# Performance work log

Measured on AMD Instinct MI355X. Metric: run time of the kernel, lower is better.

Reference implementation:

```python
import jax, jax.numpy as jnp
import numpy as np

DY, DO, DI = 16, 256, 256
BS = 4096
EPS = 1e-6


def setup_inputs() -> dict:
    key = jax.random.key(0)
    k1, k2, k3, k4, k5 = jax.random.split(key, 5)
    k = 1.0 / float(np.sqrt(DY * DI))
    return {
        "x": jax.random.normal(k1, (DY * DI, BS), dtype=jnp.float32),
        "rms_params": jnp.ones((DY * DI,), dtype=jnp.float32)
        + 0.01 * jax.random.normal(k2, (DY * DI,), dtype=jnp.float32),
        "w_upper": jax.random.uniform(k3, (DY, DO, DI), minval=-k, maxval=k, dtype=jnp.float32),
        "w_lower": jax.random.uniform(k4, (DY, DO, DI), minval=-k, maxval=k, dtype=jnp.float32),
        "bias": jax.random.uniform(k5, (DY * DO,), minval=-k, maxval=k, dtype=jnp.float32),
    }


def reference(x, rms_params, w_upper, w_lower, bias):
    # x: (dy*di, bs) features-first layout, matching the torch op.
    dy, do, di = w_upper.shape
    bs = x.shape[1]
    # Per-column RMS factor (fc in the original op is shape (bs,)).
    fc = jax.lax.rsqrt(jnp.mean(x * x, axis=0) + EPS)  # (bs,)
    xn = x * rms_params[:, None] * fc[None, :]          # fused norm+scale
    xb = xn.reshape(dy, di, bs)
    # Dyadic structured matmul: upper acts on block d, lower on its paired
    # (reversed) block dy-1-d.
    up = jnp.einsum("doi,dib->dob", w_upper, xb)
    lo = jnp.einsum("doi,dib->dob", w_lower, xb[::-1])
    y = jax.nn.relu(up + lo + bias.reshape(dy, do, 1))
    return y.reshape(dy * do, bs)
```

## Files before the change

kernel.cpp:

```cpp
#include <hip/hip_runtime.h>

#define DYN 16
#define DON 256
#define DIN 256
#define BSN 4096
#define NF 4096
#define KTOT 512

typedef unsigned short u16;
typedef __attribute__((ext_vector_type(8))) short bf16x8;
typedef __attribute__((ext_vector_type(4))) float f32x4;
typedef __attribute__((ext_vector_type(4))) unsigned short u16x4;

static __device__ __forceinline__ u16 f2bf(float f) {
  unsigned u = __builtin_bit_cast(unsigned, f);
  u += 0x7fffu + ((u >> 16) & 1u);
  return (u16)(u >> 16);
}
static __device__ __forceinline__ float bf2f(u16 h) {
  unsigned u = ((unsigned)h) << 16;
  return __builtin_bit_cast(float, u);
}

__global__ __launch_bounds__(256) void k_pre(
    const float* __restrict__ x, const float* __restrict__ wu,
    const float* __restrict__ wl, const float* __restrict__ rms,
    u16* __restrict__ aprep, u16* __restrict__ xbf,
    float* __restrict__ partial) {
  __shared__ u16 tile[128 * 132];
  const int t = threadIdx.x;
  if (blockIdx.x < 1024) {
    int e = blockIdx.x * 256 + t;
    int row = e >> 6;
    int k0 = (e & 63) << 3;
    int d = row >> 8;
    const float* src;
    const float* rp;
    if (k0 < 256) {
      src = wu + (size_t)row * 256 + k0;
      rp  = rms + d * 256 + k0;
    } else {
      src = wl + (size_t)row * 256 + (k0 - 256);
      rp  = rms + (DYN - 1 - d) * 256 + (k0 - 256);
    }
    float4 s0 = *reinterpret_cast<const float4*>(src);
    float4 s1 = *reinterpret_cast<const float4*>(src + 4);
    float4 r0 = *reinterpret_cast<const float4*>(rp);
    float4 r1 = *reinterpret_cast<const float4*>(rp + 4);
    bf16x8 o;
    o[0] = (short)f2bf(s0.x * r0.x); o[1] = (short)f2bf(s0.y * r0.y);
    o[2] = (short)f2bf(s0.z * r0.z); o[3] = (short)f2bf(s0.w * r0.w);
    o[4] = (short)f2bf(s1.x * r1.x); o[5] = (short)f2bf(s1.y * r1.y);
    o[6] = (short)f2bf(s1.z * r1.z); o[7] = (short)f2bf(s1.w * r1.w);
    *reinterpret_cast<bf16x8*>(aprep + (size_t)row * KTOT + k0) = o;
    return;
  }
  const int bid = blockIdx.x - 1024;
  const int bt = bid & 31, ft = bid >> 5;
  const float* xb = x + (size_t)ft * 128 * BSN + bt * 128;
  const int frow = t >> 5, b4 = (t & 31) * 4;
  #pragma unroll
  for (int p = 0; p < 16; ++p) {
    int f = p * 8 + frow;
    float4 v = *reinterpret_cast<const float4*>(xb + (size_t)f * BSN + b4);
    u16x4 h;
    h[0] = f2bf(v.x); h[1] = f2bf(v.y); h[2] = f2bf(v.z); h[3] = f2bf(v.w);
    *reinterpret_cast<u16x4*>(&tile[f * 132 + b4]) = h;
  }
  __syncthreads();
  const int chunk = t & 15;
  const int bg = t >> 4;
  #pragma unroll
  for (int p = 0; p < 8; ++p) {
    int b = bg + p * 16;
    float s = 0.f;
    bf16x8 w;
    #pragma unroll
    for (int jj = 0; jj < 8; ++jj) {
      int j = (jj + chunk) & 7;
      u16 v = tile[(chunk * 8 + j) * 132 + b];
      float xv = bf2f(v);
      s += xv * xv;
      w[j] = (short)v;
    }
    *reinterpret_cast<bf16x8*>(
        xbf + (size_t)(bt * 128 + b) * NF + ft * 128 + chunk * 8) = w;
    #pragma unroll
    for (int m = 1; m < 16; m <<= 1) s += __shfl_xor(s, m, 64);
    if (chunk == 0) partial[ft * BSN + bt * 128 + b] = s;
  }
}

__global__ __launch_bounds__(512, 2) void k_gemm(
    const u16* __restrict__ aprep, const u16* __restrict__ xbf,
    const float* __restrict__ partial, const float* __restrict__ bias,
    float* __restrict__ out) {
  extern __shared__ char smem[];
  float* fcl = (float*)(smem + 98304);
  const int bid = blockIdx.x;
  const int dp = bid & 7;
  const int d = ((bid >> 3) & 1) ? (15 - dp) : dp;
  const int bt = bid >> 4;
  const int b0 = bt * 256;
  const int fr0 = d * 256;
  const int t = threadIdx.x;
  const int wave = t >> 6, lane = t & 63;
  const int lhi = lane >> 4, llo = lane & 15;
  const int wm = wave >> 2, wn = wave & 3;
  const int kmask = ((llo >> 1) & 7) << 4;

  f32x4 acc[8][4] = {};

  auto stage1 = [&](int slot, int kt, int op) {
    int j = op & 1;
    int c = j * 512 + t;
    int cl = c ^ ((c >> 3) & 7);
    int r = cl >> 2, kc = cl & 3;
    unsigned lbase = (unsigned)(slot * 32768 + (op >= 2 ? 16384 : 0) +
                                (j * 512 + wave * 64) * 16);
    const u16* g;
    if (op < 2) {
      int fbase = (kt < 8) ? (d * 256 + kt * 32)
                           : ((15 - d) * 256 + (kt - 8) * 32);
      g = xbf + (size_t)(b0 + r) * NF + fbase + kc * 8;
    } else {
      g = aprep + (size_t)(fr0 + r) * KTOT + kt * 32 + kc * 8;
    }
    __builtin_amdgcn_global_load_lds(
        (const __attribute__((address_space(1))) unsigned int*)g,
        (__attribute__((address_space(3))) unsigned int*)(smem + lbase),
        16, 0, 0);
  };
  auto stageK = [&](int slot, int kt) {
    #pragma unroll
    for (int op = 0; op < 4; ++op) stage1(slot, kt, op);
  };

  if (t < 256) {
    float fs = 0.f;
    #pragma unroll
    for (int i = 0; i < 32; ++i) fs += partial[i * BSN + b0 + t];
    fcl[t] = rsqrtf(fs * (1.0f / 4096.0f) + 1e-6f);
  }
  stageK(0, 0);
  stageK(1, 1);
  asm volatile("s_waitcnt vmcnt(4)\n\ts_barrier" ::: "memory");

  for (int kt = 0; kt < 16; ++kt) {
    const int slot = kt % 3;
    const char* sA = (const char*)smem + slot * 32768;
    const char* sB = sA + 16384;
    const int st_slot = (kt + 2) % 3;
    const bool do_st = kt < 14;
    bf16x8 af[4], bf0[2], bf1[2];

    #pragma unroll
    for (int i = 0; i < 4; ++i) {
      int row = wm * 128 + i * 16 + llo;
      af[i] = *reinterpret_cast<const bf16x8*>(sA + ((row * 64 + lhi * 16) ^ kmask));
    }
    #pragma unroll
    for (int j = 0; j < 2; ++j) {
      int row = wn * 64 + j * 16 + llo;
      bf0[j] = *reinterpret_cast<const bf16x8*>(sB + ((row * 64 + lhi * 16) ^ kmask));
    }
    if (do_st) stage1(st_slot, kt + 2, 0);
    asm volatile("" ::: "memory");
    __builtin_amdgcn_s_barrier();
    __builtin_amdgcn_s_setprio(1);
    #pragma unroll
    for (int i = 0; i < 4; ++i)
      #pragma unroll
      for (int j = 0; j < 2; ++j)
        acc[i][j] = __builtin_amdgcn_mfma_f32_16x16x32_bf16(af[i], bf0[j], acc[i][j], 0, 0, 0);
    __builtin_amdgcn_s_setprio(0);
    asm volatile("" ::: "memory");
    __builtin_amdgcn_s_barrier();

    #pragma unroll
    for (int j = 0; j < 2; ++j) {
      int row = wn * 64 + 32 + j * 16 + llo;
      bf1[j] = *reinterpret_cast<const bf16x8*>(sB + ((row * 64 + lhi * 16) ^ kmask));
    }
    if (do_st) stage1(st_slot, kt + 2, 1);
    asm volatile("" ::: "memory");
    __builtin_amdgcn_s_barrier();
    __builtin_amdgcn_s_setprio(1);
    #pragma unroll
    for (int i = 0; i < 4; ++i)
      #pragma unroll
      for (int j = 0; j < 2; ++j)
        acc[i][2 + j] = __builtin_amdgcn_mfma_f32_16x16x32_bf16(af[i], bf1[j], acc[i][2 + j], 0, 0, 0);
    __builtin_amdgcn_s_setprio(0);
    asm volatile("" ::: "memory");
    __builtin_amdgcn_s_barrier();

    #pragma unroll
    for (int i = 0; i < 4; ++i) {
      int row = wm * 128 + 64 + i * 16 + llo;
      af[i] = *reinterpret_cast<const bf16x8*>(sA + ((row * 64 + lhi * 16) ^ kmask));
    }
    if (do_st) stage1(st_slot, kt + 2, 2);
    asm volatile("" ::: "memory");
    __builtin_amdgcn_s_barrier();
    __builtin_amdgcn_s_setprio(1);
    #pragma unroll
    for (int i = 0; i < 4; ++i)
      #pragma unroll
      for (int j = 0; j < 2; ++j)
        acc[4 + i][j] = __builtin_amdgcn_mfma_f32_16x16x32_bf16(af[i], bf0[j], acc[4 + i][j], 0, 0, 0);
    __builtin_amdgcn_s_setprio(0);
    asm volatile("" ::: "memory");
    __builtin_amdgcn_s_barrier();

    if (do_st) stage1(st_slot, kt + 2, 3);
    __builtin_amdgcn_s_setprio(1);
    #pragma unroll
    for (int i = 0; i < 4; ++i)
      #pragma unroll
      for (int j = 0; j < 2; ++j)
        acc[4 + i][2 + j] = __builtin_amdgcn_mfma_f32_16x16x32_bf16(af[i], bf1[j], acc[4 + i][2 + j], 0, 0, 0);
    __builtin_amdgcn_s_setprio(0);
    if (kt < 14) {
      asm volatile("s_waitcnt vmcnt(4)\n\ts_barrier" ::: "memory");
    } else if (kt == 14) {
      asm volatile("s_waitcnt vmcnt(0)\n\ts_barrier" ::: "memory");
    }
  }

  #pragma unroll
  for (int m = 0; m < 8; ++m) {
    int lb = wm * 128 + m * 16 + lhi * 4;
    float4 fq = *reinterpret_cast<const float4*>(&fcl[lb]);
    #pragma unroll
    for (int n = 0; n < 4; ++n) {
      int fo = fr0 + wn * 64 + n * 16 + llo;
      float bv = bias[fo];
      float4 v;
      v.x = fmaxf(acc[m][n][0] * fq.x + bv, 0.f);
      v.y = fmaxf(acc[m][n][1] * fq.y + bv, 0.f);
      v.z = fmaxf(acc[m][n][2] * fq.z + bv, 0.f);
      v.w = fmaxf(acc[m][n][3] * fq.w + bv, 0.f);
      *reinterpret_cast<float4*>(out + (size_t)fo * BSN + b0 + lb) = v;
    }
  }
}

extern "C" void kernel_launch(void* const* d_in, const int* in_sizes, int n_in,
                              void* d_out, int out_size, void* d_ws, size_t ws_size,
                              hipStream_t stream) {
  (void)in_sizes; (void)n_in; (void)out_size; (void)ws_size;
  const float* x    = (const float*)d_in[0];
  const float* rms  = (const float*)d_in[1];
  const float* wu   = (const float*)d_in[2];
  const float* wl   = (const float*)d_in[3];
  const float* bias = (const float*)d_in[4];
  float* out = (float*)d_out;

  char* ws = (char*)d_ws;
  u16* xbf      = (u16*)ws;
  u16* aprep    = (u16*)(ws + 33554432);
  float* partial = (float*)(ws + 37748736);

  k_pre<<<2048, 256, 0, stream>>>(x, wu, wl, rms, aprep, xbf, partial);
  k_gemm<<<256, 512, 99328, stream>>>(aprep, xbf, partial, bias, out);
}
```

Baseline: 54.69 us.

## Merge MFMA phases into two halves and stage epilogue through LDS for coalesced stores

The main loop now loads all four B fragments up front and runs two MFMA phases per k-step instead of four, issuing two global-to-LDS staging chunks per phase. This halves the number of barriers per iteration at the cost of holding more fragment registers. The epilogue writes each wave's tile to a padded LDS scratch area and reads it back so that global stores are contiguous 256-byte rows rather than scattered 16-byte pieces. The write-back adds a __syncthreads and extra LDS traffic.

```diff
diff --git a/kernel.cpp b/kernel.cpp
--- a/kernel.cpp
+++ b/kernel.cpp
@@ -152,74 +152,45 @@
     const char* sB = sA + 16384;
     const int st_slot = (kt + 2) % 3;
     const bool do_st = kt < 14;
-    bf16x8 af[4], bf0[2], bf1[2];
-
+    bf16x8 af[4], bfr[4];
+
+    #pragma unroll
+    for (int j = 0; j < 4; ++j) {
+      int row = wn * 64 + j * 16 + llo;
+      bfr[j] = *reinterpret_cast<const bf16x8*>(sB + ((row * 64 + lhi * 16) ^ kmask));
+    }
     #pragma unroll
     for (int i = 0; i < 4; ++i) {
       int row = wm * 128 + i * 16 + llo;
       af[i] = *reinterpret_cast<const bf16x8*>(sA + ((row * 64 + lhi * 16) ^ kmask));
     }
-    #pragma unroll
-    for (int j = 0; j < 2; ++j) {
-      int row = wn * 64 + j * 16 + llo;
-      bf0[j] = *reinterpret_cast<const bf16x8*>(sB + ((row * 64 + lhi * 16) ^ kmask));
-    }
-    if (do_st) stage1(st_slot, kt + 2, 0);
+    if (do_st) { stage1(st_slot, kt + 2, 0); stage1(st_slot, kt + 2, 1); }
     asm volatile("" ::: "memory");
     __builtin_amdgcn_s_barrier();
     __builtin_amdgcn_s_setprio(1);
     #pragma unroll
     for (int i = 0; i < 4; ++i)
       #pragma unroll
-      for (int j = 0; j < 2; ++j)
-        acc[i][j] = __builtin_amdgcn_mfma_f32_16x16x32_bf16(af[i], bf0[j], acc[i][j], 0, 0, 0);
+      for (int j = 0; j < 4; ++j)
+        acc[i][j] = __builtin_amdgcn_mfma_f32_16x16x32_bf16(af[i], bfr[j], acc[i][j], 0, 0, 0);
     __builtin_amdgcn_s_setprio(0);
     asm volatile("" ::: "memory");
     __builtin_amdgcn_s_barrier();
 
     #pragma unroll
-    for (int j = 0; j < 2; ++j) {
-      int row = wn * 64 + 32 + j * 16 + llo;
-      bf1[j] = *reinterpret_cast<const bf16x8*>(sB + ((row * 64 + lhi * 16) ^ kmask));
-    }
-    if (do_st) stage1(st_slot, kt + 2, 1);
+    for (int i = 0; i < 4; ++i) {
+      int row = wm * 128 + 64 + i * 16 + llo;
+      af[i] = *reinterpret_cast<const bf16x8*>(sA + ((row * 64 + lhi * 16) ^ kmask));
+    }
+    if (do_st) { stage1(st_slot, kt + 2, 2); stage1(st_slot, kt + 2, 3); }
     asm volatile("" ::: "memory");
     __builtin_amdgcn_s_barrier();
     __builtin_amdgcn_s_setprio(1);
     #pragma unroll
     for (int i = 0; i < 4; ++i)
       #pragma unroll
-      for (int j = 0; j < 2; ++j)
-        acc[i][2 + j] = __builtin_amdgcn_mfma_f32_16x16x32_bf16(af[i], bf1[j], acc[i][2 + j], 0, 0, 0);
-    __builtin_amdgcn_s_setprio(0);
-    asm volatile("" ::: "memory");
-    __builtin_amdgcn_s_barrier();
-
-    #pragma unroll
-    for (int i = 0; i < 4; ++i) {
-      int row = wm * 128 + 64 + i * 16 + llo;
-      af[i] = *reinterpret_cast<const bf16x8*>(sA + ((row * 64 + lhi * 16) ^ kmask));
-    }
-    if (do_st) stage1(st_slot, kt + 2, 2);
-    asm volatile("" ::: "memory");
-    __builtin_amdgcn_s_barrier();
-    __builtin_amdgcn_s_setprio(1);
-    #pragma unroll
-    for (int i = 0; i < 4; ++i)
-      #pragma unroll
-      for (int j = 0; j < 2; ++j)
-        acc[4 + i][j] = __builtin_amdgcn_mfma_f32_16x16x32_bf16(af[i], bf0[j], acc[4 + i][j], 0, 0, 0);
-    __builtin_amdgcn_s_setprio(0);
-    asm volatile("" ::: "memory");
-    __builtin_amdgcn_s_barrier();
-
-    if (do_st) stage1(st_slot, kt + 2, 3);
-    __builtin_amdgcn_s_setprio(1);
-    #pragma unroll
-    for (int i = 0; i < 4; ++i)
-      #pragma unroll
-      for (int j = 0; j < 2; ++j)
-        acc[4 + i][2 + j] = __builtin_amdgcn_mfma_f32_16x16x32_bf16(af[i], bf1[j], acc[4 + i][2 + j], 0, 0, 0);
+      for (int j = 0; j < 4; ++j)
+        acc[4 + i][j] = __builtin_amdgcn_mfma_f32_16x16x32_bf16(af[i], bfr[j], acc[4 + i][j], 0, 0, 0);
     __builtin_amdgcn_s_setprio(0);
     if (kt < 14) {
       asm volatile("s_waitcnt vmcnt(4)\n\ts_barrier" ::: "memory");
@@ -228,20 +199,31 @@
     }
   }
 
+  __syncthreads();
+  float* esc = (float*)smem + wave * 2112;
   #pragma unroll
-  for (int m = 0; m < 8; ++m) {
-    int lb = wm * 128 + m * 16 + lhi * 4;
-    float4 fq = *reinterpret_cast<const float4*>(&fcl[lb]);
-    #pragma unroll
-    for (int n = 0; n < 4; ++n) {
-      int fo = fr0 + wn * 64 + n * 16 + llo;
-      float bv = bias[fo];
+  for (int n = 0; n < 4; ++n) {
+    int fo_l = wn * 64 + n * 16;
+    float bv = bias[fr0 + fo_l + llo];
+    #pragma unroll
+    for (int m = 0; m < 8; ++m) {
+      int lb = wm * 128 + m * 16 + lhi * 4;
+      float4 fq = *reinterpret_cast<const float4*>(&fcl[lb]);
       float4 v;
       v.x = fmaxf(acc[m][n][0] * fq.x + bv, 0.f);
       v.y = fmaxf(acc[m][n][1] * fq.y + bv, 0.f);
       v.z = fmaxf(acc[m][n][2] * fq.z + bv, 0.f);
       v.w = fmaxf(acc[m][n][3] * fq.w + bv, 0.f);
-      *reinterpret_cast<float4*>(out + (size_t)fo * BSN + b0 + lb) = v;
+      *reinterpret_cast<float4*>(&esc[llo * 132 + m * 16 + lhi * 4]) = v;
+    }
+    #pragma unroll
+    for (int g = 0; g < 4; ++g) {
+      int fl = g * 4 + lhi;
+      size_t ob = (size_t)(fr0 + fo_l + fl) * BSN + b0 + wm * 128 + llo * 4;
+      float4 v0 = *reinterpret_cast<const float4*>(&esc[fl * 132 + llo * 4]);
+      float4 v1 = *reinterpret_cast<const float4*>(&esc[fl * 132 + 64 + llo * 4]);
+      *reinterpret_cast<float4*>(out + ob) = v0;
+      *reinterpret_cast<float4*>(out + ob + 64) = v1;
     }
   }
 }
```

New measurement: 55.92 us. 2.2% more time.
